# Kernel optimization log

Measured on AMD Instinct MI355X. Metric: run time of the kernel, lower is better.

## Reference

```python
import jax, jax.numpy as jnp
import numpy as np

D = 1024        # embed_dim
H = 16          # num_heads
HD = D // H     # head_dim
R = 8           # LoRA rank
LORA_SCALE = 16.0 / R  # alpha / r
W_BITS = 8
A_BITS = 8


def fake_quant(x, bits):
    # symmetric per-tensor fake quantization with straight-through estimator
    qmax = 2.0 ** (bits - 1) - 1.0
    scale = jnp.maximum(jnp.max(jnp.abs(x)) / qmax, 1e-8)
    q = jnp.round(x / scale) * scale
    return x + jax.lax.stop_gradient(q - x)


def quant_lora_linear(x, W, b, A, B):
    # QuantizeLinear: fake-quant activations (a_bits) and weights (w_bits)
    base = jnp.matmul(fake_quant(x, A_BITS), fake_quant(W, W_BITS).T) + b
    # active LoRA adapter: x @ A^T @ B^T * scaling (dropout=0)
    lora = jnp.matmul(jnp.matmul(x, A.T), B.T) * LORA_SCALE
    return base + lora


def setup_inputs() -> dict:
    key = jax.random.key(0)
    ks = jax.random.split(key, 20)
    bsz, seq = 2, 2048
    inp = {
        "hidden_states": jax.random.normal(ks[0], (bsz, seq, D), jnp.float32),
        "attention_mask": jnp.ones((bsz, seq), jnp.float32),
    }
    i = 1
    for name in ("q", "k", "v", "out"):
        inp[f"{name}_W"] = jax.random.normal(ks[i], (D, D), jnp.float32) * 0.02; i += 1
        inp[f"{name}_b"] = jnp.zeros((D,), jnp.float32)
        inp[f"{name}_A"] = jax.random.normal(ks[i], (R, D), jnp.float32) * 0.01; i += 1
        inp[f"{name}_B"] = jax.random.normal(ks[i], (D, R), jnp.float32) * 0.01; i += 1
    return inp


def reference(hidden_states, attention_mask,
              q_W, q_b, q_A, q_B,
              k_W, k_b, k_A, k_B,
              v_W, v_b, v_A, v_B,
              out_W, out_b, out_A, out_B):
    bsz, seq, _ = hidden_states.shape

    q = quant_lora_linear(hidden_states, q_W, q_b, q_A, q_B)
    k = quant_lora_linear(hidden_states, k_W, k_b, k_A, k_B)
    v = quant_lora_linear(hidden_states, v_W, v_b, v_A, v_B)

    # (b, s, D) -> (b, H, s, HD)
    def shape_heads(x):
        return x.reshape(bsz, seq, H, HD).transpose(0, 2, 1, 3)

    q, k, v = shape_heads(q), shape_heads(k), shape_heads(v)

    scores = jnp.einsum("bhqd,bhkd->bhqk", q, k) / jnp.sqrt(jnp.float32(HD))
    # additive mask: (1 - mask) * -10000, broadcast over (b, 1, 1, s)
    scores = scores + (1.0 - attention_mask)[:, None, None, :] * -10000.0
    probs = jax.nn.softmax(scores, axis=-1)

    attn = jnp.einsum("bhqk,bhkd->bhqd", probs, v)
    attn = attn.transpose(0, 2, 1, 3).reshape(bsz, seq, D)
    return quant_lora_linear(attn, out_W, out_b, out_A, out_B)
```

## Files before the change

### kernel.cpp

```cpp
#include <hip/hip_runtime.h>
#include <stdint.h>

typedef __attribute__((ext_vector_type(8))) short short8;
typedef __attribute__((ext_vector_type(4))) float f32x4;
typedef __attribute__((ext_vector_type(4))) int int32x4;
typedef unsigned short ushort_t;
typedef signed char i8_t;

#define SEQ   2048
#define BSZ   2
#define DIM   1024
#define NHEAD 16
#define HDIM  64
#define MROWS (BSZ*SEQ)

__device__ __forceinline__ ushort_t f2bf(float f) {
  unsigned u = __float_as_uint(f);
  unsigned r = u + 0x7fffu + ((u >> 16) & 1u);
  return (ushort_t)(r >> 16);
}

__device__ __forceinline__ unsigned cvt_pk_bf16(float lo, float hi) {
  unsigned r;
  asm("v_cvt_pk_bf16_f32 %0, %1, %2" : "=v"(r) : "v"(lo), "v"(hi));
  return r;
}

__device__ __forceinline__ float fast_exp2(float x) {
#if __has_builtin(__builtin_amdgcn_exp2f)
  return __builtin_amdgcn_exp2f(x);
#else
  return exp2f(x);
#endif
}

__device__ __forceinline__ int pack4i8(float a, float b, float c, float d) {
  int ia = (int)rintf(a), ib = (int)rintf(b), ic = (int)rintf(c), id = (int)rintf(d);
  return (ia & 255) | ((ib & 255) << 8) | ((ic & 255) << 16) | (id << 24);
}

typedef __attribute__((address_space(1))) void gas_void;
typedef __attribute__((address_space(3))) void las_void;
__device__ __forceinline__ void gll16(const void* g, void* l, int lane) {
#if __has_builtin(__builtin_amdgcn_global_load_lds)
  __builtin_amdgcn_global_load_lds((gas_void*)g, (las_void*)l, 16, 0, 0);
#else
  ((int4*)l)[lane] = *(const int4*)g;
#endif
}

__device__ __forceinline__ void amax_reduce_store(float m, unsigned* slot) {
  __shared__ float wred[4];
  int wv = threadIdx.x >> 6, lane = threadIdx.x & 63;
#pragma unroll
  for (int off = 32; off > 0; off >>= 1) m = fmaxf(m, __shfl_down(m, off));
  if (lane == 0) wred[wv] = m;
  __syncthreads();
  if (threadIdx.x == 0) {
    float r = fmaxf(fmaxf(wred[0], wred[1]), fmaxf(wred[2], wred[3]));
    atomicMax(slot, __float_as_uint(r));
  }
}

__global__ __launch_bounds__(256) void amax5_kernel(
    const float* __restrict__ x, const float* w0, const float* w1,
    const float* w2, const float* w3, int n4x, int n4w,
    unsigned* __restrict__ slots) {
  int y = blockIdx.y;
  const float* p = (y == 0) ? x : (y == 1) ? w0 : (y == 2) ? w1 : (y == 3) ? w2 : w3;
  int n4 = (y == 0) ? n4x : n4w;
  const float4* x4 = (const float4*)p;
  float m = 0.f;
  for (int i = blockIdx.x * blockDim.x + threadIdx.x; i < n4; i += gridDim.x * blockDim.x) {
    float4 v = x4[i];
    m = fmaxf(m, fmaxf(fmaxf(fabsf(v.x), fabsf(v.y)), fmaxf(fabsf(v.z), fabsf(v.w))));
  }
  amax_reduce_store(m, slots + y);
}

__global__ __launch_bounds__(256) void prep_kernel(
    const float* __restrict__ x, const unsigned* __restrict__ slots,
    i8_t* __restrict__ xc,
    const float* __restrict__ A0, const float* __restrict__ A1, const float* __restrict__ A2,
    float* __restrict__ t0, float* __restrict__ t1, float* __restrict__ t2,
    const float* w0, const float* w1, const float* w2, const float* w3,
    i8_t* q0, i8_t* q1, i8_t* q2, i8_t* q3, int n4w) {
  const int tid = threadIdx.x;
  if ((int)blockIdx.x >= MROWS) {
    int wb = blockIdx.x - MROWS;
    int y = wb >> 7, bx = wb & 127;
    const float* wsrc = (y == 0) ? w0 : (y == 1) ? w1 : (y == 2) ? w2 : w3;
    i8_t* qc = (y == 0) ? q0 : (y == 1) ? q1 : (y == 2) ? q2 : q3;
    float amax = __uint_as_float(slots[y + 1]);
    float inv = 1.0f / fmaxf(amax / 127.0f, 1e-8f);
    const float4* x4 = (const float4*)wsrc;
    int* q4 = (int*)qc;
    for (int i = bx * 256 + tid; i < n4w; i += 128 * 256) {
      float4 v = x4[i];
      q4[i] = pack4i8(v.x * inv, v.y * inv, v.z * inv, v.w * inv);
    }
    return;
  }
  const int row = blockIdx.x;
  const int k0 = tid * 4;
  float amax = __uint_as_float(slots[0]);
  float inv = 1.0f / fmaxf(amax / 127.0f, 1e-8f);

  float4 xv = *(const float4*)&x[(size_t)row * DIM + k0];
  *(int*)&xc[(size_t)row * DIM + k0] = pack4i8(xv.x * inv, xv.y * inv, xv.z * inv, xv.w * inv);

  float p[24];
#pragma unroll
  for (int r = 0; r < 8; r++) {
    float4 a = *(const float4*)&A0[r * DIM + k0];
    p[r] = xv.x * a.x + xv.y * a.y + xv.z * a.z + xv.w * a.w;
    float4 a1 = *(const float4*)&A1[r * DIM + k0];
    p[8 + r] = xv.x * a1.x + xv.y * a1.y + xv.z * a1.z + xv.w * a1.w;
    float4 a2 = *(const float4*)&A2[r * DIM + k0];
    p[16 + r] = xv.x * a2.x + xv.y * a2.y + xv.z * a2.z + xv.w * a2.w;
  }
#pragma unroll
  for (int j = 0; j < 24; j++) {
    float v = p[j];
#pragma unroll
    for (int off = 32; off > 0; off >>= 1) v += __shfl_down(v, off);
    p[j] = v;
  }
  __shared__ float red[4][24];
  int wv = tid >> 6, lane = tid & 63;
  if (lane == 0) {
#pragma unroll
    for (int j = 0; j < 24; j++) red[wv][j] = p[j];
  }
  __syncthreads();
  if (tid < 24) {
    int j = tid;
    float sv = red[0][j] + red[1][j] + red[2][j] + red[3][j];
    float* tp = (j < 8) ? t0 : ((j < 16) ? t1 : t2);
    tp[(size_t)row * 8 + (j & 7)] = sv;
  }
}

__global__ __launch_bounds__(256) void lora_quant1_kernel(
    const float* __restrict__ x, const unsigned* __restrict__ slot,
    i8_t* __restrict__ xc, const float* __restrict__ A0, float* __restrict__ t0) {
  const int row = blockIdx.x;
  const int tid = threadIdx.x;
  const int k0 = tid * 4;
  float amax = __uint_as_float(*slot);
  float inv = 1.0f / fmaxf(amax / 127.0f, 1e-8f);

  float4 xv = *(const float4*)&x[(size_t)row * DIM + k0];
  *(int*)&xc[(size_t)row * DIM + k0] = pack4i8(xv.x * inv, xv.y * inv, xv.z * inv, xv.w * inv);

  float p[8];
#pragma unroll
  for (int r = 0; r < 8; r++) {
    float4 a = *(const float4*)&A0[r * DIM + k0];
    p[r] = xv.x * a.x + xv.y * a.y + xv.z * a.z + xv.w * a.w;
  }
#pragma unroll
  for (int j = 0; j < 8; j++) {
    float v = p[j];
#pragma unroll
    for (int off = 32; off > 0; off >>= 1) v += __shfl_down(v, off);
    p[j] = v;
  }
  __shared__ float red[4][8];
  int wv = tid >> 6, lane = tid & 63;
  if (lane == 0) {
#pragma unroll
    for (int j = 0; j < 8; j++) red[wv][j] = p[j];
  }
  __syncthreads();
  if (tid < 8) {
    int j = tid;
    t0[(size_t)row * 8 + j] = red[0][j] + red[1][j] + red[2][j] + red[3][j];
  }
}

template <bool BF16OUT, int BN, bool CANTRANS>
__device__ __forceinline__ void proj_body(
    const i8_t* __restrict__ Ac, const i8_t* __restrict__ Wc,
    const unsigned* __restrict__ sxslot, const unsigned* __restrict__ swslot,
    const float* __restrict__ bias, const float* __restrict__ t,
    const float* __restrict__ Bl, void* __restrict__ Cout,
    ushort_t* __restrict__ vTout, int m0, int n0) {
  constexpr int CODEB = 128 * 128 + BN * 128;
  constexpr int T2B = CANTRANS ? 128 * 136 * 2 : 0;
  constexpr int BASE = (T2B > CODEB) ? T2B : CODEB;
  __shared__ alignas(16) char smem[BASE + 128 * 32 + BN * 32 + BN * 4];
  i8_t* Asb = (i8_t*)smem;
  i8_t* Bsb = (i8_t*)(smem + 128 * 128);
  ushort_t* T2 = (ushort_t*)smem;
  float* Ts = (float*)(smem + BASE);
  float* Bls = Ts + 128 * 8;
  float* biass = Bls + BN * 8;

  const int tid = threadIdx.x;
  constexpr int NJ = BN / 32;
  constexpr int BITS = BN / 32;

  for (int i = tid; i < 128 * 8; i += 256) Ts[i] = t[(size_t)m0 * 8 + i];
  for (int i = tid; i < BN * 8; i += 256) Bls[i] = Bl[(size_t)n0 * 8 + i];
  if (tid < BN) biass[tid] = bias[n0 + tid];

  int32x4 acc[4][NJ];
#pragma unroll
  for (int i = 0; i < 4; i++)
#pragma unroll
    for (int j = 0; j < NJ; j++) {
      acc[i][j][0] = 0; acc[i][j][1] = 0; acc[i][j][2] = 0; acc[i][j][3] = 0;
    }

  const int wv = tid >> 6, lane = tid & 63;
  const int wr = wv >> 1, wc = wv & 1;
  const int l15 = lane & 15, hi = lane >> 4;
  const int lr8 = lane >> 3, lc8 = lane & 7;

  for (int kt = 0; kt < 8; kt++) {
    const int k0 = kt * 128;
#pragma unroll
    for (int j = 0; j < 4; j++) {
      int row = wv * 32 + j * 8 + lr8;
      int cs = lc8 ^ (row & 7);
      gll16(&Ac[(size_t)(m0 + row) * DIM + k0 + cs * 16], &Asb[(wv * 32 + j * 8) * 128], lane);
    }
#pragma unroll
    for (int j = 0; j < BITS; j++) {
      int row = wv * (BN / 4) + j * 8 + lr8;
      int cs = lc8 ^ (row & 7);
      gll16(&Wc[(size_t)(n0 + row) * DIM + k0 + cs * 16], &Bsb[(wv * (BN / 4) + j * 8) * 128], lane);
    }
    __syncthreads();
#pragma unroll
    for (int ks = 0; ks < 2; ks++) {
      int32x4 a[4], b[NJ];
#pragma unroll
      for (int i = 0; i < 4; i++) {
        int row = wr * 64 + i * 16 + l15;
        a[i] = *(const int32x4*)&Asb[row * 128 + (((ks * 4 + hi) ^ (row & 7))) * 16];
      }
#pragma unroll
      for (int j = 0; j < NJ; j++) {
        int col = wc * (BN / 2) + j * 16 + l15;
        b[j] = *(const int32x4*)&Bsb[col * 128 + (((ks * 4 + hi) ^ (col & 7))) * 16];
      }
      __builtin_amdgcn_s_setprio(1);
#pragma unroll
      for (int i = 0; i < 4; i++)
#pragma unroll
        for (int j = 0; j < NJ; j++)
          acc[i][j] = __builtin_amdgcn_mfma_i32_16x16x64_i8(a[i], b[j], acc[i][j], 0, 0, 0);
      __builtin_amdgcn_s_setprio(0);
    }
    __syncthreads();
  }

  float sx = fmaxf(__uint_as_float(*sxslot) / 127.0f, 1e-8f);
  float sw = fmaxf(__uint_as_float(*swslot) / 127.0f, 1e-8f);
  float ss = sx * sw;

  if (CANTRANS && vTout != nullptr) {
#pragma unroll
    for (int i = 0; i < 4; i++) {
      int rl0 = wr * 64 + i * 16 + hi * 4;
      float tv[4][8];
#pragma unroll
      for (int rr = 0; rr < 4; rr++)
#pragma unroll
        for (int q = 0; q < 8; q++) tv[rr][q] = Ts[(rl0 + rr) * 8 + q];
#pragma unroll
      for (int j = 0; j < NJ; j++) {
        int cl = wc * (BN / 2) + j * 16 + l15;
        float val[4];
#pragma unroll
        for (int rr = 0; rr < 4; rr++) {
          float lr = 0.f;
#pragma unroll
          for (int q = 0; q < 8; q++) lr += tv[rr][q] * Bls[cl * 8 + q];
          val[rr] = (float)acc[i][j][rr] * ss + biass[cl] + 2.0f * lr;
        }
        unsigned w0 = cvt_pk_bf16(val[0], val[1]);
        unsigned w1 = cvt_pk_bf16(val[2], val[3]);
        *(uint2*)&T2[cl * 136 + rl0] = make_uint2(w0, w1);
      }
    }
    __syncthreads();
    const int bb = m0 >> 11;
    const int sbase = m0 & 2047;
#pragma unroll
    for (int it = 0; it < 8; it++) {
      int g = it * 256 + tid;
      int d = g >> 4, c = g & 15;
      int gdim = n0 + d;
      int hh = gdim >> 6, dd = gdim & 63;
      int bh = bb * 16 + hh;
      int4 v = *(const int4*)&T2[d * 136 + c * 8];
      *(int4*)&vTout[((size_t)(bh * 64 + dd)) * SEQ + sbase + c * 8] = v;
    }
    return;
  }

#pragma unroll
  for (int i = 0; i < 4; i++) {
#pragma unroll
    for (int rr = 0; rr < 4; rr++) {
      int rl = wr * 64 + i * 16 + hi * 4 + rr;
      float tv[8];
#pragma unroll
      for (int q = 0; q < 8; q++) tv[q] = Ts[rl * 8 + q];
#pragma unroll
      for (int j = 0; j < NJ; j++) {
        int cl = wc * (BN / 2) + j * 16 + l15;
        float lr = 0.f;
#pragma unroll
        for (int q = 0; q < 8; q++) lr += tv[q] * Bls[cl * 8 + q];
        float val = (float)acc[i][j][rr] * ss + biass[cl] + 2.0f * lr;
        if (BF16OUT)
          ((ushort_t*)Cout)[(size_t)(m0 + rl) * DIM + n0 + cl] = f2bf(val);
        else
          ((float*)Cout)[(size_t)(m0 + rl) * DIM + n0 + cl] = val;
      }
    }
  }
}

struct ProjSet {
  const i8_t* W; const unsigned* sw; const float* bias;
  const float* t; const float* Bl; ushort_t* out;
};

__global__ __launch_bounds__(256) void proj_qkv_kernel(
    const i8_t* __restrict__ Ac, const unsigned* __restrict__ sxslot,
    ProjSet pq, ProjSet pk, ProjSet pv, ushort_t* __restrict__ vT) {
  ProjSet P = (blockIdx.z == 0) ? pq : (blockIdx.z == 1) ? pk : pv;
  ushort_t* vt = (blockIdx.z == 2) ? vT : nullptr;
  proj_body<true, 128, true>(Ac, P.W, sxslot, P.sw, P.bias, P.t, P.Bl, P.out,
                             vt, blockIdx.y * 128, blockIdx.x * 128);
}

__global__ __launch_bounds__(256) void proj_out_kernel(
    const i8_t* __restrict__ Ac, const i8_t* __restrict__ Wc,
    const unsigned* __restrict__ sxslot, const unsigned* __restrict__ swslot,
    const float* __restrict__ bias, const float* __restrict__ t,
    const float* __restrict__ Bl, float* __restrict__ Cout) {
  proj_body<false, 64, false>(Ac, Wc, sxslot, swslot, bias, t, Bl, Cout,
                              nullptr, blockIdx.y * 128, blockIdx.x * 64);
}

__global__ __launch_bounds__(256) void attn9_kernel(
    const ushort_t* __restrict__ qb, const ushort_t* __restrict__ kb,
    const ushort_t* __restrict__ vT, const float* __restrict__ mask,
    float* __restrict__ obuf, unsigned* __restrict__ amax_slot) {
  __shared__ alignas(16) ushort_t Ks[2][64 * 64];
  __shared__ alignas(16) ushort_t Vs[2][64 * 64];
  __shared__ alignas(16) ushort_t Ps[128 * 72];
  __shared__ alignas(16) float maskv[2][64];
  __shared__ float wmax[4];

  const float LOG2E = 1.44269504088896f;
  const float SCL2 = 0.125f * LOG2E;
  const float THR2 = 8.0f * LOG2E;

  const int lin = blockIdx.x;
  const int logical = (lin & 7) * 64 + (lin >> 3);
  const int bh = logical >> 4;
  const int qt = logical & 15;
  const int b = bh >> 4, h = bh & 15;
  const size_t tokbase = (size_t)b * SEQ;
  const int q0 = qt * 128;

  const int tid = threadIdx.x;
  const int wv = tid >> 6, lane = tid & 63, l15 = lane & 15, hi = lane >> 4;
  const int sr = tid >> 3, sc = tid & 7;
  const int sslot = (sc ^ (sr & 7)) * 8;
  const int sslot2 = (sc ^ ((sr + 32) & 7)) * 8;

  short8 qf[2][2];
#pragma unroll
  for (int rb = 0; rb < 2; rb++)
#pragma unroll
    for (int ks = 0; ks < 2; ks++) {
      int row = q0 + wv * 32 + rb * 16 + l15;
      qf[rb][ks] = *(const short8*)&qb[(tokbase + row) * DIM + h * 64 + ks * 32 + hi * 8];
    }

  float mo[2], ls[2];
  f32x4 o[2][4];
#pragma unroll
  for (int rb = 0; rb < 2; rb++) { mo[rb] = -1e30f; ls[rb] = 0.f; }
#pragma unroll
  for (int rb = 0; rb < 2; rb++)
#pragma unroll
    for (int d = 0; d < 4; d++) { o[rb][d][0] = 0.f; o[rb][d][1] = 0.f; o[rb][d][2] = 0.f; o[rb][d][3] = 0.f; }

  int4 kpre0, kpre1, vpre0, vpre1;
  float mpre;
  kpre0 = *(const int4*)&kb[(tokbase + sr) * DIM + h * 64 + sc * 8];
  vpre0 = *(const int4*)&vT[((size_t)bh * 64 + sr) * SEQ + sc * 8];
  kpre1 = *(const int4*)&kb[(tokbase + sr + 32) * DIM + h * 64 + sc * 8];
  vpre1 = *(const int4*)&vT[((size_t)bh * 64 + sr + 32) * SEQ + sc * 8];
  mpre = (tid < 64) ? (1.0f - mask[tokbase + tid]) * (-10000.0f * LOG2E) : 0.f;
  *(int4*)&Ks[0][sr * 64 + sslot] = kpre0;
  *(int4*)&Vs[0][sr * 64 + sslot] = vpre0;
  *(int4*)&Ks[0][(sr + 32) * 64 + sslot2] = kpre1;
  *(int4*)&Vs[0][(sr + 32) * 64 + sslot2] = vpre1;
  if (tid < 64) maskv[0][tid] = mpre;
  __syncthreads();

  for (int kt = 0; kt < 32; kt++) {
    const int cur = kt & 1, nxt = cur ^ 1;

    if (kt < 31) {
      const int k0n = (kt + 1) * 64;
      kpre0 = *(const int4*)&kb[(tokbase + k0n + sr) * DIM + h * 64 + sc * 8];
      vpre0 = *(const int4*)&vT[((size_t)bh * 64 + sr) * SEQ + k0n + sc * 8];
      kpre1 = *(const int4*)&kb[(tokbase + k0n + sr + 32) * DIM + h * 64 + sc * 8];
      vpre1 = *(const int4*)&vT[((size_t)bh * 64 + sr + 32) * SEQ + k0n + sc * 8];
      if (tid < 64) mpre = (1.0f - mask[tokbase + k0n + tid]) * (-10000.0f * LOG2E);
    }

    f32x4 s2[4][2];
#pragma unroll
    for (int kb4 = 0; kb4 < 4; kb4++)
#pragma unroll
      for (int rb = 0; rb < 2; rb++) { s2[kb4][rb][0] = 0.f; s2[kb4][rb][1] = 0.f; s2[kb4][rb][2] = 0.f; s2[kb4][rb][3] = 0.f; }
#pragma unroll
    for (int ks = 0; ks < 2; ks++) {
      short8 kf[4];
#pragma unroll
      for (int kb4 = 0; kb4 < 4; kb4++) {
        int row = kb4 * 16 + l15;
        kf[kb4] = *(const short8*)&Ks[cur][row * 64 + (((ks * 4 + hi) ^ (row & 7))) * 8];
      }
      __builtin_amdgcn_s_setprio(1);
#pragma unroll
      for (int kb4 = 0; kb4 < 4; kb4++)
#pragma unroll
        for (int rb = 0; rb < 2; rb++)
          s2[kb4][rb] = __builtin_amdgcn_mfma_f32_16x16x32_bf16(kf[kb4], qf[rb][ks], s2[kb4][rb], 0, 0, 0);
      __builtin_amdgcn_s_setprio(0);
    }

#pragma unroll
    for (int kb4 = 0; kb4 < 4; kb4++) {
      f32x4 mkv = *(const f32x4*)&maskv[cur][kb4 * 16 + hi * 4];
#pragma unroll
      for (int rb = 0; rb < 2; rb++)
#pragma unroll
        for (int r = 0; r < 4; r++)
          s2[kb4][rb][r] = s2[kb4][rb][r] * SCL2 + mkv[r];
    }

    float tm[2];
#pragma unroll
    for (int rb = 0; rb < 2; rb++) {
      float t0m = fmaxf(fmaxf(s2[0][rb][0], s2[0][rb][1]), fmaxf(s2[0][rb][2], s2[0][rb][3]));
      float t1m = fmaxf(fmaxf(s2[1][rb][0], s2[1][rb][1]), fmaxf(s2[1][rb][2], s2[1][rb][3]));
      float t2m = fmaxf(fmaxf(s2[2][rb][0], s2[2][rb][1]), fmaxf(s2[2][rb][2], s2[2][rb][3]));
      float t3m = fmaxf(fmaxf(s2[3][rb][0], s2[3][rb][1]), fmaxf(s2[3][rb][2], s2[3][rb][3]));
      float t = fmaxf(fmaxf(t0m, t1m), fmaxf(t2m, t3m));
      t = fmaxf(t, __shfl_xor(t, 16));
      t = fmaxf(t, __shfl_xor(t, 32));
      tm[rb] = t;
    }

    bool need = (tm[0] > mo[0] + THR2) || (tm[1] > mo[1] + THR2);
    if (__any(need)) {
      float al[2];
#pragma unroll
      for (int rb = 0; rb < 2; rb++) {
        float mn = fmaxf(mo[rb], tm[rb]);
        al[rb] = fast_exp2(mo[rb] - mn);
        mo[rb] = mn;
        ls[rb] *= al[rb];
      }
#pragma unroll
      for (int rb = 0; rb < 2; rb++)
#pragma unroll
        for (int r = 0; r < 4; r++) {
          float ab = __shfl(al[rb], hi * 4 + r);
#pragma unroll
          for (int db = 0; db < 4; db++) o[rb][db][r] *= ab;
        }
    }

#pragma unroll
    for (int rb = 0; rb < 2; rb++) {
      float rsv = 0.f;
#pragma unroll
      for (int kb4 = 0; kb4 < 4; kb4++)
#pragma unroll
        for (int r = 0; r < 4; r++) {
          float pv = fast_exp2(s2[kb4][rb][r] - mo[rb]);
          s2[kb4][rb][r] = pv;
          rsv += pv;
        }
      rsv += __shfl_xor(rsv, 16);
      rsv += __shfl_xor(rsv, 32);
      ls[rb] += rsv;
    }

#pragma unroll
    for (int rb = 0; rb < 2; rb++) {
      int rowb = (wv * 32 + rb * 16 + l15) * 72;
#pragma unroll
      for (int kb4 = 0; kb4 < 4; kb4++) {
        unsigned w0 = cvt_pk_bf16(s2[kb4][rb][0], s2[kb4][rb][1]);
        unsigned w1 = cvt_pk_bf16(s2[kb4][rb][2], s2[kb4][rb][3]);
        *(uint2*)&Ps[rowb + kb4 * 16 + hi * 4] = make_uint2(w0, w1);
      }
    }

#pragma unroll
    for (int ks = 0; ks < 2; ks++) {
      short8 pf[2];
#pragma unroll
      for (int rb = 0; rb < 2; rb++) {
        int row = wv * 32 + rb * 16 + l15;
        pf[rb] = *(const short8*)&Ps[row * 72 + ks * 32 + hi * 8];
      }
      short8 vf[4];
#pragma unroll
      for (int db = 0; db < 4; db++) {
        int row = db * 16 + l15;
        vf[db] = *(const short8*)&Vs[cur][row * 64 + (((ks * 4 + hi) ^ (row & 7))) * 8];
      }
      __builtin_amdgcn_s_setprio(1);
#pragma unroll
      for (int rb = 0; rb < 2; rb++)
#pragma unroll
        for (int db = 0; db < 4; db++)
          o[rb][db] = __builtin_amdgcn_mfma_f32_16x16x32_bf16(pf[rb], vf[db], o[rb][db], 0, 0, 0);
      __builtin_amdgcn_s_setprio(0);
    }

    if (kt < 31) {
      *(int4*)&Ks[nxt][sr * 64 + sslot] = kpre0;
      *(int4*)&Vs[nxt][sr * 64 + sslot] = vpre0;
      *(int4*)&Ks[nxt][(sr + 32) * 64 + sslot2] = kpre1;
      *(int4*)&Vs[nxt][(sr + 32) * 64 + sslot2] = vpre1;
      if (tid < 64) maskv[nxt][tid] = mpre;
    }
    __syncthreads();
  }

  float am = 0.f;
#pragma unroll
  for (int rb = 0; rb < 2; rb++)
#pragma unroll
    for (int r = 0; r < 4; r++) {
      float lsb = __shfl(ls[rb], hi * 4 + r);
      float inv = 1.0f / lsb;
      size_t row = tokbase + q0 + wv * 32 + rb * 16 + hi * 4 + r;
#pragma unroll
      for (int db = 0; db < 4; db++) {
        float val = o[rb][db][r] * inv;
        am = fmaxf(am, fabsf(val));
        obuf[row * DIM + h * 64 + db * 16 + l15] = val;
      }
    }
#pragma unroll
  for (int off = 32; off > 0; off >>= 1) am = fmaxf(am, __shfl_down(am, off));
  if (lane == 0) wmax[wv] = am;
  __syncthreads();
  if (tid == 0)
    atomicMax(amax_slot, __float_as_uint(fmaxf(fmaxf(wmax[0], wmax[1]), fmaxf(wmax[2], wmax[3]))));
}

extern "C" void kernel_launch(void* const* d_in, const int* in_sizes, int n_in,
                              void* d_out, int out_size, void* d_ws, size_t ws_size,
                              hipStream_t stream) {
  const float* x     = (const float*)d_in[0];
  const float* mask  = (const float*)d_in[1];
  const float* q_W   = (const float*)d_in[2];
  const float* q_b   = (const float*)d_in[3];
  const float* q_A   = (const float*)d_in[4];
  const float* q_B   = (const float*)d_in[5];
  const float* k_W   = (const float*)d_in[6];
  const float* k_b   = (const float*)d_in[7];
  const float* k_A   = (const float*)d_in[8];
  const float* k_B   = (const float*)d_in[9];
  const float* v_W   = (const float*)d_in[10];
  const float* v_b   = (const float*)d_in[11];
  const float* v_A   = (const float*)d_in[12];
  const float* v_B   = (const float*)d_in[13];
  const float* o_W   = (const float*)d_in[14];
  const float* o_b   = (const float*)d_in[15];
  const float* o_A   = (const float*)d_in[16];
  const float* o_B   = (const float*)d_in[17];
  float* out = (float*)d_out;

  char* ws = (char*)d_ws;
  const size_t MB = 1u << 20;
  unsigned* slots = (unsigned*)ws;
  float* t_q = (float*)(ws + 4096);
  float* t_k = t_q + MROWS * 8;
  float* t_v = t_k + MROWS * 8;
  float* t_o = t_v + MROWS * 8;
  i8_t* xc  = (i8_t*)(ws + 1 * MB);
  i8_t* qWc = (i8_t*)(ws + 9 * MB);
  i8_t* kWc = (i8_t*)(ws + 11 * MB);
  i8_t* vWc = (i8_t*)(ws + 13 * MB);
  i8_t* oWc = (i8_t*)(ws + 15 * MB);
  ushort_t* qbb = (ushort_t*)(ws + 17 * MB);
  ushort_t* kbb = (ushort_t*)(ws + 25 * MB);
  ushort_t* vTb = (ushort_t*)(ws + 41 * MB);
  float*    abuf = (float*)(ws + 49 * MB);
  i8_t*     ac  = (i8_t*)(ws + 65 * MB);

  (void)hipMemsetAsync(ws, 0, 64, stream);

  const int NX4 = (MROWS * DIM) / 4;
  const int NW4 = (DIM * DIM) / 4;

  amax5_kernel<<<dim3(256, 5), 256, 0, stream>>>(x, q_W, k_W, v_W, o_W, NX4, NW4, slots);

  prep_kernel<<<MROWS + 512, 256, 0, stream>>>(x, slots, xc, q_A, k_A, v_A,
                                               t_q, t_k, t_v,
                                               q_W, k_W, v_W, o_W,
                                               qWc, kWc, vWc, oWc, NW4);

  ProjSet pq = { qWc, slots + 1, q_b, t_q, q_B, qbb };
  ProjSet pk = { kWc, slots + 2, k_b, t_k, k_B, kbb };
  ProjSet pv = { vWc, slots + 3, v_b, t_v, v_B, nullptr };
  proj_qkv_kernel<<<dim3(DIM / 128, MROWS / 128, 3), 256, 0, stream>>>(
      xc, slots + 0, pq, pk, pv, vTb);

  attn9_kernel<<<512, 256, 0, stream>>>(qbb, kbb, vTb, mask, abuf, slots + 5);

  lora_quant1_kernel<<<MROWS, 256, 0, stream>>>(abuf, slots + 5, ac, o_A, t_o);

  proj_out_kernel<<<dim3(DIM / 64, MROWS / 128), 256, 0, stream>>>(
      ac, oWc, slots + 5, slots + 4, o_b, t_o, o_B, out);
}
```

Before: 184.2 us.

## Use 8 waves per attention block and store attention output as bf16

The attention kernel now launches 512 threads per block, so each wave handles 16 query rows instead of 32. Each thread loads one K and one V vector per tile instead of two. The attention output buffer changes from fp32 to bf16, halving the intermediate write and read, and the LoRA/quant kernel reads it as bf16. This trades more waves per block (fewer registers per wave) for lower per-wave latency, and adds bf16 rounding of the attention output before fake quantization, which can change numerics.

```diff
diff --git a/kernel.cpp b/kernel.cpp
--- a/kernel.cpp
+++ b/kernel.cpp
@@ -18,6 +18,9 @@
   unsigned u = __float_as_uint(f);
   unsigned r = u + 0x7fffu + ((u >> 16) & 1u);
   return (ushort_t)(r >> 16);
+}
+__device__ __forceinline__ float bf2f(ushort_t u) {
+  return __uint_as_float(((unsigned)u) << 16);
 }
 
 __device__ __forceinline__ unsigned cvt_pk_bf16(float lo, float hi) {
@@ -142,7 +145,7 @@
 }
 
 __global__ __launch_bounds__(256) void lora_quant1_kernel(
-    const float* __restrict__ x, const unsigned* __restrict__ slot,
+    const ushort_t* __restrict__ x, const unsigned* __restrict__ slot,
     i8_t* __restrict__ xc, const float* __restrict__ A0, float* __restrict__ t0) {
   const int row = blockIdx.x;
   const int tid = threadIdx.x;
@@ -150,14 +153,15 @@
   float amax = __uint_as_float(*slot);
   float inv = 1.0f / fmaxf(amax / 127.0f, 1e-8f);
 
-  float4 xv = *(const float4*)&x[(size_t)row * DIM + k0];
-  *(int*)&xc[(size_t)row * DIM + k0] = pack4i8(xv.x * inv, xv.y * inv, xv.z * inv, xv.w * inv);
+  ushort4 xu = *(const ushort4*)&x[(size_t)row * DIM + k0];
+  float xv0 = bf2f(xu.x), xv1 = bf2f(xu.y), xv2 = bf2f(xu.z), xv3 = bf2f(xu.w);
+  *(int*)&xc[(size_t)row * DIM + k0] = pack4i8(xv0 * inv, xv1 * inv, xv2 * inv, xv3 * inv);
 
   float p[8];
 #pragma unroll
   for (int r = 0; r < 8; r++) {
     float4 a = *(const float4*)&A0[r * DIM + k0];
-    p[r] = xv.x * a.x + xv.y * a.y + xv.z * a.z + xv.w * a.w;
+    p[r] = xv0 * a.x + xv1 * a.y + xv2 * a.z + xv3 * a.w;
   }
 #pragma unroll
   for (int j = 0; j < 8; j++) {
@@ -349,15 +353,15 @@
                               nullptr, blockIdx.y * 128, blockIdx.x * 64);
 }
 
-__global__ __launch_bounds__(256) void attn9_kernel(
+__global__ __launch_bounds__(512) void attn10_kernel(
     const ushort_t* __restrict__ qb, const ushort_t* __restrict__ kb,
     const ushort_t* __restrict__ vT, const float* __restrict__ mask,
-    float* __restrict__ obuf, unsigned* __restrict__ amax_slot) {
+    ushort_t* __restrict__ obuf, unsigned* __restrict__ amax_slot) {
   __shared__ alignas(16) ushort_t Ks[2][64 * 64];
   __shared__ alignas(16) ushort_t Vs[2][64 * 64];
   __shared__ alignas(16) ushort_t Ps[128 * 72];
   __shared__ alignas(16) float maskv[2][64];
-  __shared__ float wmax[4];
+  __shared__ float wmax[8];
 
   const float LOG2E = 1.44269504088896f;
   const float SCL2 = 0.125f * LOG2E;
@@ -375,37 +379,26 @@
   const int wv = tid >> 6, lane = tid & 63, l15 = lane & 15, hi = lane >> 4;
   const int sr = tid >> 3, sc = tid & 7;
   const int sslot = (sc ^ (sr & 7)) * 8;
-  const int sslot2 = (sc ^ ((sr + 32) & 7)) * 8;
-
-  short8 qf[2][2];
-#pragma unroll
-  for (int rb = 0; rb < 2; rb++)
-#pragma unroll
-    for (int ks = 0; ks < 2; ks++) {
-      int row = q0 + wv * 32 + rb * 16 + l15;
-      qf[rb][ks] = *(const short8*)&qb[(tokbase + row) * DIM + h * 64 + ks * 32 + hi * 8];
-    }
-
-  float mo[2], ls[2];
-  f32x4 o[2][4];
-#pragma unroll
-  for (int rb = 0; rb < 2; rb++) { mo[rb] = -1e30f; ls[rb] = 0.f; }
-#pragma unroll
-  for (int rb = 0; rb < 2; rb++)
-#pragma unroll
-    for (int d = 0; d < 4; d++) { o[rb][d][0] = 0.f; o[rb][d][1] = 0.f; o[rb][d][2] = 0.f; o[rb][d][3] = 0.f; }
-
-  int4 kpre0, kpre1, vpre0, vpre1;
+
+  short8 qf[2];
+#pragma unroll
+  for (int ks = 0; ks < 2; ks++) {
+    int row = q0 + wv * 16 + l15;
+    qf[ks] = *(const short8*)&qb[(tokbase + row) * DIM + h * 64 + ks * 32 + hi * 8];
+  }
+
+  float mo = -1e30f, ls = 0.f;
+  f32x4 o[4];
+#pragma unroll
+  for (int d = 0; d < 4; d++) { o[d][0] = 0.f; o[d][1] = 0.f; o[d][2] = 0.f; o[d][3] = 0.f; }
+
+  int4 kpre, vpre;
   float mpre;
-  kpre0 = *(const int4*)&kb[(tokbase + sr) * DIM + h * 64 + sc * 8];
-  vpre0 = *(const int4*)&vT[((size_t)bh * 64 + sr) * SEQ + sc * 8];
-  kpre1 = *(const int4*)&kb[(tokbase + sr + 32) * DIM + h * 64 + sc * 8];
-  vpre1 = *(const int4*)&vT[((size_t)bh * 64 + sr + 32) * SEQ + sc * 8];
+  kpre = *(const int4*)&kb[(tokbase + sr) * DIM + h * 64 + sc * 8];
+  vpre = *(const int4*)&vT[((size_t)bh * 64 + sr) * SEQ + sc * 8];
   mpre = (tid < 64) ? (1.0f - mask[tokbase + tid]) * (-10000.0f * LOG2E) : 0.f;
-  *(int4*)&Ks[0][sr * 64 + sslot] = kpre0;
-  *(int4*)&Vs[0][sr * 64 + sslot] = vpre0;
-  *(int4*)&Ks[0][(sr + 32) * 64 + sslot2] = kpre1;
-  *(int4*)&Vs[0][(sr + 32) * 64 + sslot2] = vpre1;
+  *(int4*)&Ks[0][sr * 64 + sslot] = kpre;
+  *(int4*)&Vs[0][sr * 64 + sslot] = vpre;
   if (tid < 64) maskv[0][tid] = mpre;
   __syncthreads();
 
@@ -414,18 +407,14 @@
 
     if (kt < 31) {
       const int k0n = (kt + 1) * 64;
-      kpre0 = *(const int4*)&kb[(tokbase + k0n + sr) * DIM + h * 64 + sc * 8];
-      vpre0 = *(const int4*)&vT[((size_t)bh * 64 + sr) * SEQ + k0n + sc * 8];
-      kpre1 = *(const int4*)&kb[(tokbase + k0n + sr + 32) * DIM + h * 64 + sc * 8];
-      vpre1 = *(const int4*)&vT[((size_t)bh * 64 + sr + 32) * SEQ + k0n + sc * 8];
+      kpre = *(const int4*)&kb[(tokbase + k0n + sr) * DIM + h * 64 + sc * 8];
+      vpre = *(const int4*)&vT[((size_t)bh * 64 + sr) * SEQ + k0n + sc * 8];
       if (tid < 64) mpre = (1.0f - mask[tokbase + k0n + tid]) * (-10000.0f * LOG2E);
     }
 
-    f32x4 s2[4][2];
-#pragma unroll
-    for (int kb4 = 0; kb4 < 4; kb4++)
-#pragma unroll
-      for (int rb = 0; rb < 2; rb++) { s2[kb4][rb][0] = 0.f; s2[kb4][rb][1] = 0.f; s2[kb4][rb][2] = 0.f; s2[kb4][rb][3] = 0.f; }
+    f32x4 s2[4];
+#pragma unroll
+    for (int kb4 = 0; kb4 < 4; kb4++) { s2[kb4][0] = 0.f; s2[kb4][1] = 0.f; s2[kb4][2] = 0.f; s2[kb4][3] = 0.f; }
 #pragma unroll
     for (int ks = 0; ks < 2; ks++) {
       short8 kf[4];
@@ -437,9 +426,7 @@
       __builtin_amdgcn_s_setprio(1);
 #pragma unroll
       for (int kb4 = 0; kb4 < 4; kb4++)
-#pragma unroll
-        for (int rb = 0; rb < 2; rb++)
-          s2[kb4][rb] = __builtin_amdgcn_mfma_f32_16x16x32_bf16(kf[kb4], qf[rb][ks], s2[kb4][rb], 0, 0, 0);
+        s2[kb4] = __builtin_amdgcn_mfma_f32_16x16x32_bf16(kf[kb4], qf[ks], s2[kb4], 0, 0, 0);
       __builtin_amdgcn_s_setprio(0);
     }
 
@@ -447,80 +434,58 @@
     for (int kb4 = 0; kb4 < 4; kb4++) {
       f32x4 mkv = *(const f32x4*)&maskv[cur][kb4 * 16 + hi * 4];
 #pragma unroll
-      for (int rb = 0; rb < 2; rb++)
-#pragma unroll
-        for (int r = 0; r < 4; r++)
-          s2[kb4][rb][r] = s2[kb4][rb][r] * SCL2 + mkv[r];
-    }
-
-    float tm[2];
-#pragma unroll
-    for (int rb = 0; rb < 2; rb++) {
-      float t0m = fmaxf(fmaxf(s2[0][rb][0], s2[0][rb][1]), fmaxf(s2[0][rb][2], s2[0][rb][3]));
-      float t1m = fmaxf(fmaxf(s2[1][rb][0], s2[1][rb][1]), fmaxf(s2[1][rb][2], s2[1][rb][3]));
-      float t2m = fmaxf(fmaxf(s2[2][rb][0], s2[2][rb][1]), fmaxf(s2[2][rb][2], s2[2][rb][3]));
-      float t3m = fmaxf(fmaxf(s2[3][rb][0], s2[3][rb][1]), fmaxf(s2[3][rb][2], s2[3][rb][3]));
-      float t = fmaxf(fmaxf(t0m, t1m), fmaxf(t2m, t3m));
-      t = fmaxf(t, __shfl_xor(t, 16));
-      t = fmaxf(t, __shfl_xor(t, 32));
-      tm[rb] = t;
-    }
-
-    bool need = (tm[0] > mo[0] + THR2) || (tm[1] > mo[1] + THR2);
+      for (int r = 0; r < 4; r++)
+        s2[kb4][r] = s2[kb4][r] * SCL2 + mkv[r];
+    }
+
+    float t0m = fmaxf(fmaxf(s2[0][0], s2[0][1]), fmaxf(s2[0][2], s2[0][3]));
+    float t1m = fmaxf(fmaxf(s2[1][0], s2[1][1]), fmaxf(s2[1][2], s2[1][3]));
+    float t2m = fmaxf(fmaxf(s2[2][0], s2[2][1]), fmaxf(s2[2][2], s2[2][3]));
+    float t3m = fmaxf(fmaxf(s2[3][0], s2[3][1]), fmaxf(s2[3][2], s2[3][3]));
+    float tm = fmaxf(fmaxf(t0m, t1m), fmaxf(t2m, t3m));
+    tm = fmaxf(tm, __shfl_xor(tm, 16));
+    tm = fmaxf(tm, __shfl_xor(tm, 32));
+
+    bool need = (tm > mo + THR2);
     if (__any(need)) {
-      float al[2];
-#pragma unroll
-      for (int rb = 0; rb < 2; rb++) {
-        float mn = fmaxf(mo[rb], tm[rb]);
-        al[rb] = fast_exp2(mo[rb] - mn);
-        mo[rb] = mn;
-        ls[rb] *= al[rb];
-      }
-#pragma unroll
-      for (int rb = 0; rb < 2; rb++)
-#pragma unroll
-        for (int r = 0; r < 4; r++) {
-          float ab = __shfl(al[rb], hi * 4 + r);
-#pragma unroll
-          for (int db = 0; db < 4; db++) o[rb][db][r] *= ab;
-        }
-    }
-
-#pragma unroll
-    for (int rb = 0; rb < 2; rb++) {
-      float rsv = 0.f;
-#pragma unroll
-      for (int kb4 = 0; kb4 < 4; kb4++)
-#pragma unroll
-        for (int r = 0; r < 4; r++) {
-          float pv = fast_exp2(s2[kb4][rb][r] - mo[rb]);
-          s2[kb4][rb][r] = pv;
-          rsv += pv;
-        }
-      rsv += __shfl_xor(rsv, 16);
-      rsv += __shfl_xor(rsv, 32);
-      ls[rb] += rsv;
-    }
-
-#pragma unroll
-    for (int rb = 0; rb < 2; rb++) {
-      int rowb = (wv * 32 + rb * 16 + l15) * 72;
+      float mn = fmaxf(mo, tm);
+      float al = fast_exp2(mo - mn);
+      mo = mn;
+      ls *= al;
+#pragma unroll
+      for (int r = 0; r < 4; r++) {
+        float ab = __shfl(al, hi * 4 + r);
+#pragma unroll
+        for (int db = 0; db < 4; db++) o[db][r] *= ab;
+      }
+    }
+
+    float rsv = 0.f;
+#pragma unroll
+    for (int kb4 = 0; kb4 < 4; kb4++)
+#pragma unroll
+      for (int r = 0; r < 4; r++) {
+        float pv = fast_exp2(s2[kb4][r] - mo);
+        s2[kb4][r] = pv;
+        rsv += pv;
+      }
+    rsv += __shfl_xor(rsv, 16);
+    rsv += __shfl_xor(rsv, 32);
+    ls += rsv;
+
+    {
+      int rowb = (wv * 16 + l15) * 72;
 #pragma unroll
       for (int kb4 = 0; kb4 < 4; kb4++) {
-        unsigned w0 = cvt_pk_bf16(s2[kb4][rb][0], s2[kb4][rb][1]);
-        unsigned w1 = cvt_pk_bf16(s2[kb4][rb][2], s2[kb4][rb][3]);
+        unsigned w0 = cvt_pk_bf16(s2[kb4][0], s2[kb4][1]);
+        unsigned w1 = cvt_pk_bf16(s2[kb4][2], s2[kb4][3]);
         *(uint2*)&Ps[rowb + kb4 * 16 + hi * 4] = make_uint2(w0, w1);
       }
     }
 
 #pragma unroll
     for (int ks = 0; ks < 2; ks++) {
-      short8 pf[2];
-#pragma unroll
-      for (int rb = 0; rb < 2; rb++) {
-        int row = wv * 32 + rb * 16 + l15;
-        pf[rb] = *(const short8*)&Ps[row * 72 + ks * 32 + hi * 8];
-      }
+      short8 pf = *(const short8*)&Ps[(wv * 16 + l15) * 72 + ks * 32 + hi * 8];
       short8 vf[4];
 #pragma unroll
       for (int db = 0; db < 4; db++) {
@@ -529,18 +494,14 @@
       }
       __builtin_amdgcn_s_setprio(1);
 #pragma unroll
-      for (int rb = 0; rb < 2; rb++)
-#pragma unroll
-        for (int db = 0; db < 4; db++)
-          o[rb][db] = __builtin_amdgcn_mfma_f32_16x16x32_bf16(pf[rb], vf[db], o[rb][db], 0, 0, 0);
+      for (int db = 0; db < 4; db++)
+        o[db] = __builtin_amdgcn_mfma_f32_16x16x32_bf16(pf, vf[db], o[db], 0, 0, 0);
       __builtin_amdgcn_s_setprio(0);
     }
 
     if (kt < 31) {
-      *(int4*)&Ks[nxt][sr * 64 + sslot] = kpre0;
-      *(int4*)&Vs[nxt][sr * 64 + sslot] = vpre0;
-      *(int4*)&Ks[nxt][(sr + 32) * 64 + sslot2] = kpre1;
-      *(int4*)&Vs[nxt][(sr + 32) * 64 + sslot2] = vpre1;
+      *(int4*)&Ks[nxt][sr * 64 + sslot] = kpre;
+      *(int4*)&Vs[nxt][sr * 64 + sslot] = vpre;
       if (tid < 64) maskv[nxt][tid] = mpre;
     }
     __syncthreads();
@@ -548,25 +509,28 @@
 
   float am = 0.f;
 #pragma unroll
-  for (int rb = 0; rb < 2; rb++)
-#pragma unroll
-    for (int r = 0; r < 4; r++) {
-      float lsb = __shfl(ls[rb], hi * 4 + r);
-      float inv = 1.0f / lsb;
-      size_t row = tokbase + q0 + wv * 32 + rb * 16 + hi * 4 + r;
-#pragma unroll
-      for (int db = 0; db < 4; db++) {
-        float val = o[rb][db][r] * inv;
-        am = fmaxf(am, fabsf(val));
-        obuf[row * DIM + h * 64 + db * 16 + l15] = val;
-      }
-    }
+  for (int r = 0; r < 4; r++) {
+    float lsb = __shfl(ls, hi * 4 + r);
+    float inv = 1.0f / lsb;
+    size_t row = tokbase + q0 + wv * 16 + hi * 4 + r;
+#pragma unroll
+    for (int db = 0; db < 4; db++) {
+      float val = o[db][r] * inv;
+      ushort_t bv = f2bf(val);
+      am = fmaxf(am, fabsf(bf2f(bv)));
+      obuf[row * DIM + h * 64 + db * 16 + l15] = bv;
+    }
+  }
 #pragma unroll
   for (int off = 32; off > 0; off >>= 1) am = fmaxf(am, __shfl_down(am, off));
   if (lane == 0) wmax[wv] = am;
   __syncthreads();
-  if (tid == 0)
-    atomicMax(amax_slot, __float_as_uint(fmaxf(fmaxf(wmax[0], wmax[1]), fmaxf(wmax[2], wmax[3]))));
+  if (tid == 0) {
+    float r = wmax[0];
+#pragma unroll
+    for (int w = 1; w < 8; w++) r = fmaxf(r, wmax[w]);
+    atomicMax(amax_slot, __float_as_uint(r));
+  }
 }
 
 extern "C" void kernel_launch(void* const* d_in, const int* in_sizes, int n_in,
@@ -607,7 +571,7 @@
   ushort_t* qbb = (ushort_t*)(ws + 17 * MB);
   ushort_t* kbb = (ushort_t*)(ws + 25 * MB);
   ushort_t* vTb = (ushort_t*)(ws + 41 * MB);
-  float*    abuf = (float*)(ws + 49 * MB);
+  ushort_t* abuf = (ushort_t*)(ws + 49 * MB);
   i8_t*     ac  = (i8_t*)(ws + 65 * MB);
 
   (void)hipMemsetAsync(ws, 0, 64, stream);
@@ -628,7 +592,7 @@
   proj_qkv_kernel<<<dim3(DIM / 128, MROWS / 128, 3), 256, 0, stream>>>(
       xc, slots + 0, pq, pk, pv, vTb);
 
-  attn9_kernel<<<512, 256, 0, stream>>>(qbb, kbb, vTb, mask, abuf, slots + 5);
+  attn10_kernel<<<512, 512, 0, stream>>>(qbb, kbb, vTb, mask, abuf, slots + 5);
 
   lora_quant1_kernel<<<MROWS, 256, 0, stream>>>(abuf, slots + 5, ac, o_A, t_o);
 
```

Result: faster. 175.0 us (-5.0%).
